# Kernel optimization log

Hardware: AMD Instinct MI355X
Metric: run time of the kernel (lower is better)

## Reference

```python
import jax, jax.numpy as jnp
import numpy as np

R = 12          # resolution (H = W = G); L = R**3 = 1728
HEADS = 12


def setup_inputs() -> dict:
    key = jax.random.key(0)
    k1, k2, k3 = jax.random.split(key, 3)
    B, L, C = 4, R ** 3, 768
    qkv = jax.random.normal(k1, (3, B, L, C), dtype=jnp.float32)
    lepe_w = jax.random.normal(k2, (C, 1, 3, 3, 3), dtype=jnp.float32) * 0.05
    lepe_b = jax.random.normal(k3, (C,), dtype=jnp.float32) * 0.01
    return {"qkv": qkv, "lepe_w": lepe_w, "lepe_b": lepe_b}


def reference(qkv, lepe_w, lepe_b):
    # qkv: [3, B, L, C]; idx=0 => window == full volume, so attention is dense over L.
    q, k, v = qkv[0], qkv[1], qkv[2]
    B, L, C = q.shape
    hd = C // HEADS
    scale = hd ** -0.5

    # im2cswin with full-volume window preserves token order: [B, L, C] -> [B, H, L, d]
    qh = q.reshape(B, L, HEADS, hd).transpose(0, 2, 1, 3)
    kh = k.reshape(B, L, HEADS, hd).transpose(0, 2, 1, 3)

    # get_lepe: v -> [B, C, R, R, R], depthwise 3x3x3 conv (groups=C)
    v_img = v.transpose(0, 2, 1).reshape(B, C, R, R, R)
    lepe = jax.lax.conv_general_dilated(
        v_img, lepe_w, window_strides=(1, 1, 1), padding="SAME",
        dimension_numbers=("NCDHW", "OIDHW", "NCDHW"), feature_group_count=C,
    ) + lepe_b[None, :, None, None, None]
    lepe = lepe.reshape(B, HEADS, hd, L).transpose(0, 1, 3, 2)   # [B, H, L, d]
    vh = v_img.reshape(B, HEADS, hd, L).transpose(0, 1, 3, 2)    # [B, H, L, d]

    attn = jax.nn.softmax(jnp.einsum("bhqd,bhkd->bhqk", qh * scale, kh), axis=-1)
    out = jnp.einsum("bhqk,bhkd->bhqd", attn, vh) + lepe          # [B, H, L, d]

    # windows2img with full window is an inverse reshape back to [B, L, C]
    return out.transpose(0, 2, 1, 3).reshape(B, L, C)
```

## Files before the change

kernel.cpp:

```cpp
#include <hip/hip_runtime.h>

#define RR 12
#define LL 1728
#define CC 768
#define HEADS 12
#define HD 64
#define BATCH 4

typedef __attribute__((ext_vector_type(8))) short bf8;
typedef __attribute__((ext_vector_type(4))) float f4;

__device__ inline unsigned short f2bf(float x) {
  unsigned int u = __float_as_uint(x);
  return (unsigned short)((u + 0x7FFFu + ((u >> 16) & 1u)) >> 16);
}
__device__ inline unsigned short f2bfr(float x) {
  return (unsigned short)((__float_as_uint(x) + 0x8000u) >> 16);
}

__device__ inline float fast_exp2(float x) {
#if __has_builtin(__builtin_amdgcn_exp2f)
  return __builtin_amdgcn_exp2f(x);
#else
  return exp2f(x);
#endif
}

__device__ inline void gld16(const unsigned short* g, unsigned short* l) {
  __builtin_amdgcn_global_load_lds((const __attribute__((address_space(1))) unsigned int*)g,
                                   (__attribute__((address_space(3))) unsigned int*)l, 16, 0, 0);
}

#define QSCALE 0.1803368801111244f

#define NLEPE 5184
#define NPREP 1296

__global__ __launch_bounds__(256) void combined_kernel(const float* __restrict__ qkv,
                                                       const float* __restrict__ w,
                                                       const float* __restrict__ bias,
                                                       unsigned short* __restrict__ qb,
                                                       unsigned short* __restrict__ kb,
                                                       unsigned short* __restrict__ vT,
                                                       float* __restrict__ out) {
  __shared__ __align__(16) unsigned char smem[27648];
  const int bid = blockIdx.x;
  const int t = threadIdx.x;

  if (bid < NLEPE) {
    const int xg = (bid % 3) * 4;
    const int line = (bid / 3) % 144;
    const int ct = (bid / 432) % 3;
    const int b = bid / 1296;
    const int z = line / RR;
    const int y = line % RR;
    const int c0 = ct * 256;
    const int c = c0 + t;
    float* w_lds = (float*)smem;

    {
      const float* wsrc = w + (size_t)c0 * 27;
#pragma unroll
      for (int i = 0; i < 7; ++i) {
        const int idx = i * 256 + t;
        if (idx < 1728) *(float4*)&w_lds[idx * 4] = *(const float4*)&wsrc[idx * 4];
      }
    }
    __syncthreads();
    float wreg[27];
#pragma unroll
    for (int j = 0; j < 27; ++j) wreg[j] = w_lds[t * 27 + j];

    const float* vb = qkv + ((size_t)(2 * BATCH + b)) * LL * CC + c;
    const float bv = bias[c];
    float acc[4] = {bv, bv, bv, bv};

#pragma unroll
    for (int dz = -1; dz <= 1; ++dz) {
#pragma unroll
      for (int dy = -1; dy <= 1; ++dy) {
        const int zz = z + dz, yy = y + dy;
        const bool lineok = ((unsigned)zz < RR) & ((unsigned)yy < RR);
        const int base = (zz * RR + yy) * RR;
        float v6[6];
#pragma unroll
        for (int p = 0; p < 6; ++p) {
          const int xx = xg - 1 + p;
          const bool ok = lineok & ((unsigned)xx < RR);
          const int lp = ok ? base + xx : 0;
          const float vv = vb[(size_t)lp * CC];
          v6[p] = ok ? vv : 0.f;
        }
        const int jb = ((dz + 1) * 3 + (dy + 1)) * 3;
        const float wL = wreg[jb], wC = wreg[jb + 1], wR = wreg[jb + 2];
#pragma unroll
        for (int i = 0; i < 4; ++i)
          acc[i] += wL * v6[i] + wC * v6[i + 1] + wR * v6[i + 2];
      }
    }
    const size_t obase = ((size_t)b * LL + line * RR + xg) * CC + c;
#pragma unroll
    for (int i = 0; i < 4; ++i) out[obase + (size_t)i * CC] = acc[i];

  } else {
    const int p = bid - NLEPE;
    const int lt = p % 27;
    const int h = (p / 27) % HEADS;
    const int b = p / (27 * HEADS);
    unsigned short* tl = (unsigned short*)smem;

    {
      const int r0 = t >> 4;
      const int c4 = (t & 15) * 4;
#pragma unroll
      for (int pi = 0; pi < 4; ++pi) {
        const int row = lt * 64 + pi * 16 + r0;
        const size_t off = ((size_t)b * LL + row) * CC + h * HD + c4;
        const float4 qv = *(const float4*)(qkv + off);
        ushort4 oq;
        oq.x = f2bf(qv.x * QSCALE); oq.y = f2bf(qv.y * QSCALE);
        oq.z = f2bf(qv.z * QSCALE); oq.w = f2bf(qv.w * QSCALE);
        *(ushort4*)(qb + off) = oq;
        const float4 kv = *(const float4*)(qkv + (size_t)BATCH * LL * CC + off);
        ushort4 ok;
        ok.x = f2bf(kv.x); ok.y = f2bf(kv.y); ok.z = f2bf(kv.z); ok.w = f2bf(kv.w);
        *(ushort4*)(kb + off) = ok;
      }
    }

    const float* vsrc = qkv + ((size_t)(2 * BATCH + b)) * LL * CC;
#pragma unroll
    for (int it = 0; it < 4; ++it) {
      const int idx = it * 256 + t;
      const int lrow = idx >> 4;
      const int c4 = (idx & 15) * 4;
      const float4 vv = *(const float4*)(vsrc + (size_t)(lt * 64 + lrow) * CC + h * HD + c4);
      tl[(c4 + 0) * 65 + lrow] = f2bf(vv.x);
      tl[(c4 + 1) * 65 + lrow] = f2bf(vv.y);
      tl[(c4 + 2) * 65 + lrow] = f2bf(vv.z);
      tl[(c4 + 3) * 65 + lrow] = f2bf(vv.w);
    }
    __syncthreads();
#pragma unroll
    for (int it = 0; it < 4; ++it) {
      const int idx = it * 256 + t;
      const int drow = idx >> 4;
      const int u = idx & 15;
      const int s4 = u * 4;
      const int kbase = (((u >> 3) * 2 + (u & 1)) << 4) + (((u >> 1) & 3) << 2);
      ushort4 o;
      o.x = tl[drow * 65 + kbase + 0];
      o.y = tl[drow * 65 + kbase + 1];
      o.z = tl[drow * 65 + kbase + 2];
      o.w = tl[drow * 65 + kbase + 3];
      *(ushort4*)(vT + (((size_t)(b * HEADS + h) * HD + drow) * LL) + lt * 64 + s4) = o;
    }
  }
}

__global__ __launch_bounds__(512, 4) void attn_kernel(const unsigned short* __restrict__ qb,
                                                      const unsigned short* __restrict__ kb,
                                                      const unsigned short* __restrict__ vT,
                                                      float* __restrict__ out) {
  __shared__ unsigned short k_lds[3][64 * 64];
  __shared__ unsigned short v_lds[3][64 * 64];

  const int g = blockIdx.x;
  const int xcd = g & 7;
  const int ix = g >> 3;
  const int qt = ix % 7;
  const int bh = xcd * 6 + ix / 7;
  const int h = bh % HEADS;
  const int b = bh / HEADS;
  const int stg = (qt * 4) % 27;

  const int t = threadIdx.x;
  const int lane = t & 63;
  const int wave = t >> 6;
  const int m = lane & 15;
  const int quad = lane >> 4;

  bf8 qf[2][2];
#pragma unroll
  for (int sub = 0; sub < 2; ++sub) {
    int row = qt * 256 + sub * 128 + wave * 16 + m;
    row = row < LL ? row : LL - 1;
    const size_t qbase = ((size_t)(b * LL + row)) * CC + h * HD;
    qf[sub][0] = *(const bf8*)(qb + qbase + quad * 8);
    qf[sub][1] = *(const bf8*)(qb + qbase + 32 + quad * 8);
  }

  int koff, voff, ldsb;
  {
    const int cidx = wave * 64 + lane;
    const int row = cidx >> 3;
    const int sc = (cidx & 7) ^ (row & 7);
    koff = row * CC + sc * 8;
    voff = row * LL + sc * 8;
    ldsb = wave * 512;
  }

  const unsigned short* kgb = kb + (size_t)b * LL * CC + h * HD;
  const unsigned short* vgb = vT + ((size_t)(b * HEADS + h) * HD) * LL;

#define ISSUE_TILE(KT, BUF)                                                             \
  {                                                                                     \
    gld16(kgb + (size_t)(KT) * (64 * CC) + koff, &k_lds[BUF][ldsb]);                    \
    gld16(vgb + (KT) * 64 + voff, &v_lds[BUF][ldsb]);                                   \
  }

  ISSUE_TILE(stg, 0)
  {
    int k1 = stg + 1; if (k1 >= 27) k1 -= 27;
    ISSUE_TILE(k1, 1)
  }

  f4 o_acc[2][4] = {};
  float psum[2] = {0.f, 0.f};

#define ATTN_BODY(I, STG, WAITN, DOISSUE)                                               \
  {                                                                                     \
    __asm__ volatile("s_waitcnt vmcnt(" #WAITN ")" ::: "memory");                       \
    __builtin_amdgcn_s_barrier();                                                       \
    if (DOISSUE) {                                                                      \
      int ktn = stg + (I) + 2; if (ktn >= 27) ktn -= 27;                                \
      ISSUE_TILE(ktn, ((STG) + 2) % 3)                                                  \
    }                                                                                   \
    f4 s_acc[2][4] = {};                                                                \
    __builtin_amdgcn_s_setprio(1);                                                      \
    _Pragma("unroll")                                                                   \
    for (int nt = 0; nt < 4; ++nt) {                                                    \
      _Pragma("unroll")                                                                 \
      for (int ks = 0; ks < 2; ++ks) {                                                  \
        const int cc = ((ks * 4 + quad) ^ (m & 7)) * 8;                                 \
        const bf8 kf = *(const bf8*)&k_lds[STG][(nt * 16 + m) * 64 + cc];               \
        s_acc[0][nt] = __builtin_amdgcn_mfma_f32_16x16x32_bf16(kf, qf[0][ks], s_acc[0][nt], 0, 0, 0); \
        s_acc[1][nt] = __builtin_amdgcn_mfma_f32_16x16x32_bf16(kf, qf[1][ks], s_acc[1][nt], 0, 0, 0); \
      }                                                                                 \
    }                                                                                   \
    __builtin_amdgcn_s_setprio(0);                                                      \
    bf8 pf[2][2];                                                                       \
    _Pragma("unroll")                                                                   \
    for (int sub = 0; sub < 2; ++sub) {                                                 \
      _Pragma("unroll")                                                                 \
      for (int ks = 0; ks < 2; ++ks) {                                                  \
        union { bf8 v; unsigned int w[4]; } pu;                                         \
        _Pragma("unroll")                                                               \
        for (int bb = 0; bb < 2; ++bb) {                                                \
          const int nt = ks * 2 + bb;                                                   \
          const float p0 = fast_exp2(s_acc[sub][nt][0]);                                \
          const float p1 = fast_exp2(s_acc[sub][nt][1]);                                \
          const float p2 = fast_exp2(s_acc[sub][nt][2]);                                \
          const float p3 = fast_exp2(s_acc[sub][nt][3]);                                \
          psum[sub] += (p0 + p1) + (p2 + p3);                                           \
          pu.w[bb * 2 + 0] = (unsigned int)f2bfr(p0) | ((unsigned int)f2bfr(p1) << 16); \
          pu.w[bb * 2 + 1] = (unsigned int)f2bfr(p2) | ((unsigned int)f2bfr(p3) << 16); \
        }                                                                               \
        pf[sub][ks] = pu.v;                                                             \
      }                                                                                 \
    }                                                                                   \
    __builtin_amdgcn_s_setprio(1);                                                      \
    _Pragma("unroll")                                                                   \
    for (int nt = 0; nt < 4; ++nt) {                                                    \
      _Pragma("unroll")                                                                 \
      for (int ks = 0; ks < 2; ++ks) {                                                  \
        const int cc = ((ks * 4 + quad) ^ (m & 7)) * 8;                                 \
        const bf8 vf = *(const bf8*)&v_lds[STG][(nt * 16 + m) * 64 + cc];               \
        o_acc[0][nt] = __builtin_amdgcn_mfma_f32_16x16x32_bf16(vf, pf[0][ks], o_acc[0][nt], 0, 0, 0); \
        o_acc[1][nt] = __builtin_amdgcn_mfma_f32_16x16x32_bf16(vf, pf[1][ks], o_acc[1][nt], 0, 0, 0); \
      }                                                                                 \
    }                                                                                   \
    __builtin_amdgcn_s_setprio(0);                                                      \
  }

  for (int ip = 0; ip < 8; ++ip) {
    const int i0 = ip * 3;
    ATTN_BODY(i0 + 0, 0, 2, true)
    ATTN_BODY(i0 + 1, 1, 2, true)
    ATTN_BODY(i0 + 2, 2, 2, true)
  }
  ATTN_BODY(24, 0, 2, true)
  ATTN_BODY(25, 1, 2, false)
  ATTN_BODY(26, 2, 0, false)
#undef ATTN_BODY
#undef ISSUE_TILE

#pragma unroll
  for (int sub = 0; sub < 2; ++sub) {
    float s = psum[sub];
    s += __shfl_xor(s, 16);
    s += __shfl_xor(s, 32);
    const float inv = 1.0f / s;
    const int rowq = qt * 256 + sub * 128 + wave * 16 + m;
    if (rowq < LL) {
      float* op = out + ((size_t)b * LL + rowq) * CC + h * HD + quad * 4;
#pragma unroll
      for (int nt = 0; nt < 4; ++nt) {
        float4 o4 = *(float4*)&op[nt * 16];
        o4.x += o_acc[sub][nt][0] * inv;
        o4.y += o_acc[sub][nt][1] * inv;
        o4.z += o_acc[sub][nt][2] * inv;
        o4.w += o_acc[sub][nt][3] * inv;
        *(float4*)&op[nt * 16] = o4;
      }
    }
  }
}

extern "C" void kernel_launch(void* const* d_in, const int* in_sizes, int n_in,
                              void* d_out, int out_size, void* d_ws, size_t ws_size,
                              hipStream_t stream) {
  (void)in_sizes; (void)n_in; (void)ws_size; (void)out_size;
  const float* qkv = (const float*)d_in[0];
  const float* lepe_w = (const float*)d_in[1];
  const float* lepe_b = (const float*)d_in[2];
  float* out = (float*)d_out;

  const size_t NE = (size_t)BATCH * LL * CC;
  unsigned short* qb = (unsigned short*)d_ws;
  unsigned short* kb = qb + NE;
  unsigned short* vT = kb + NE;

  combined_kernel<<<dim3(NLEPE + NPREP), 256, 0, stream>>>(qkv, lepe_w, lepe_b, qb, kb, vT, out);
  attn_kernel<<<dim3(336), 512, 0, stream>>>(qb, kb, vT, out);
}
```

Baseline: 191.3 us.

## Split key tiles across wave halves and reduce partial outputs in LDS

Each block now handles 128 query rows instead of 256. The two halves of its 8 waves each process 32 of the 64 keys in every tile, and their partial output accumulators and row sums are combined through shared memory at the end. This doubles the grid to 672 blocks, cuts per-wave register use, and raises launch_bounds occupancy to 6, aiming to fill more CUs and hide latency better. In exchange it adds an LDS reduction with an extra barrier, and each K/V tile is loaded twice as often across the grid.

```diff
diff --git a/kernel.cpp b/kernel.cpp
--- a/kernel.cpp
+++ b/kernel.cpp
@@ -158,7 +158,7 @@
   }
 }
 
-__global__ __launch_bounds__(512, 4) void attn_kernel(const unsigned short* __restrict__ qb,
+__global__ __launch_bounds__(512, 6) void attn_kernel(const unsigned short* __restrict__ qb,
                                                       const unsigned short* __restrict__ kb,
                                                       const unsigned short* __restrict__ vT,
                                                       float* __restrict__ out) {
@@ -168,26 +168,28 @@
   const int g = blockIdx.x;
   const int xcd = g & 7;
   const int ix = g >> 3;
-  const int qt = ix % 7;
-  const int bh = xcd * 6 + ix / 7;
+  const int qt = ix % 14;
+  const int bh = xcd * 6 + ix / 14;
   const int h = bh % HEADS;
   const int b = bh / HEADS;
-  const int stg = (qt * 4) % 27;
+  const int stg = (qt * 2) % 27;
 
   const int t = threadIdx.x;
   const int lane = t & 63;
   const int wave = t >> 6;
   const int m = lane & 15;
   const int quad = lane >> 4;
+  const int half = wave >> 2;
+  const int qg = wave & 3;
 
   bf8 qf[2][2];
 #pragma unroll
-  for (int sub = 0; sub < 2; ++sub) {
-    int row = qt * 256 + sub * 128 + wave * 16 + m;
+  for (int qsub = 0; qsub < 2; ++qsub) {
+    int row = qt * 128 + qg * 32 + qsub * 16 + m;
     row = row < LL ? row : LL - 1;
     const size_t qbase = ((size_t)(b * LL + row)) * CC + h * HD;
-    qf[sub][0] = *(const bf8*)(qb + qbase + quad * 8);
-    qf[sub][1] = *(const bf8*)(qb + qbase + 32 + quad * 8);
+    qf[qsub][0] = *(const bf8*)(qb + qbase + quad * 8);
+    qf[qsub][1] = *(const bf8*)(qb + qbase + 32 + quad * 8);
   }
 
   int koff, voff, ldsb;
@@ -215,7 +217,7 @@
     ISSUE_TILE(k1, 1)
   }
 
-  f4 o_acc[2][4] = {};
+  f4 o_acc[4][2] = {};
   float psum[2] = {0.f, 0.f};
 
 #define ATTN_BODY(I, STG, WAITN, DOISSUE)                                               \
@@ -226,49 +228,42 @@
       int ktn = stg + (I) + 2; if (ktn >= 27) ktn -= 27;                                \
       ISSUE_TILE(ktn, ((STG) + 2) % 3)                                                  \
     }                                                                                   \
-    f4 s_acc[2][4] = {};                                                                \
+    f4 s_acc[2][2] = {};                            \
     __builtin_amdgcn_s_setprio(1);                                                      \
     _Pragma("unroll")                                                                   \
-    for (int nt = 0; nt < 4; ++nt) {                                                    \
+    for (int knt = 0; knt < 2; ++knt) {                                                 \
       _Pragma("unroll")                                                                 \
-      for (int ks = 0; ks < 2; ++ks) {                                                  \
-        const int cc = ((ks * 4 + quad) ^ (m & 7)) * 8;                                 \
-        const bf8 kf = *(const bf8*)&k_lds[STG][(nt * 16 + m) * 64 + cc];               \
-        s_acc[0][nt] = __builtin_amdgcn_mfma_f32_16x16x32_bf16(kf, qf[0][ks], s_acc[0][nt], 0, 0, 0); \
-        s_acc[1][nt] = __builtin_amdgcn_mfma_f32_16x16x32_bf16(kf, qf[1][ks], s_acc[1][nt], 0, 0, 0); \
+      for (int ksd = 0; ksd < 2; ++ksd) {                                               \
+        const int cc = ((ksd * 4 + quad) ^ (m & 7)) * 8;                                \
+        const bf8 kf = *(const bf8*)&k_lds[STG][(half * 32 + knt * 16 + m) * 64 + cc];  \
+        s_acc[knt][0] = __builtin_amdgcn_mfma_f32_16x16x32_bf16(kf, qf[0][ksd], s_acc[knt][0], 0, 0, 0); \
+        s_acc[knt][1] = __builtin_amdgcn_mfma_f32_16x16x32_bf16(kf, qf[1][ksd], s_acc[knt][1], 0, 0, 0); \
       }                                                                                 \
     }                                                                                   \
     __builtin_amdgcn_s_setprio(0);                                                      \
-    bf8 pf[2][2];                                                                       \
+    bf8 pf[2];          \
     _Pragma("unroll")                                                                   \
-    for (int sub = 0; sub < 2; ++sub) {                                                 \
+    for (int qsub = 0; qsub < 2; ++qsub) {                                              \
+      union { bf8 v; unsigned int w[4]; } pu;                                           \
       _Pragma("unroll")                                                                 \
-      for (int ks = 0; ks < 2; ++ks) {                                                  \
-        union { bf8 v; unsigned int w[4]; } pu;                                         \
-        _Pragma("unroll")                                                               \
-        for (int bb = 0; bb < 2; ++bb) {                                                \
-          const int nt = ks * 2 + bb;                                                   \
-          const float p0 = fast_exp2(s_acc[sub][nt][0]);                                \
-          const float p1 = fast_exp2(s_acc[sub][nt][1]);                                \
-          const float p2 = fast_exp2(s_acc[sub][nt][2]);                                \
-          const float p3 = fast_exp2(s_acc[sub][nt][3]);                                \
-          psum[sub] += (p0 + p1) + (p2 + p3);                                           \
-          pu.w[bb * 2 + 0] = (unsigned int)f2bfr(p0) | ((unsigned int)f2bfr(p1) << 16); \
-          pu.w[bb * 2 + 1] = (unsigned int)f2bfr(p2) | ((unsigned int)f2bfr(p3) << 16); \
-        }                                                                               \
-        pf[sub][ks] = pu.v;                                                             \
+      for (int knt = 0; knt < 2; ++knt) {                                               \
+        const float p0 = fast_exp2(s_acc[knt][qsub][0]);                                \
+        const float p1 = fast_exp2(s_acc[knt][qsub][1]);                                \
+        const float p2 = fast_exp2(s_acc[knt][qsub][2]);                                \
+        const float p3 = fast_exp2(s_acc[knt][qsub][3]);                                \
+        psum[qsub] += (p0 + p1) + (p2 + p3);                                            \
+        pu.w[knt * 2 + 0] = (unsigned int)f2bfr(p0) | ((unsigned int)f2bfr(p1) << 16);  \
+        pu.w[knt * 2 + 1] = (unsigned int)f2bfr(p2) | ((unsigned int)f2bfr(p3) << 16);  \
       }                                                                                 \
+      pf[qsub] = pu.v;                                                                  \
     }                                                                                   \
     __builtin_amdgcn_s_setprio(1);                                                      \
     _Pragma("unroll")                                                                   \
     for (int nt = 0; nt < 4; ++nt) {                                                    \
-      _Pragma("unroll")                                                                 \
-      for (int ks = 0; ks < 2; ++ks) {                                                  \
-        const int cc = ((ks * 4 + quad) ^ (m & 7)) * 8;                                 \
-        const bf8 vf = *(const bf8*)&v_lds[STG][(nt * 16 + m) * 64 + cc];               \
-        o_acc[0][nt] = __builtin_amdgcn_mfma_f32_16x16x32_bf16(vf, pf[0][ks], o_acc[0][nt], 0, 0, 0); \
-        o_acc[1][nt] = __builtin_amdgcn_mfma_f32_16x16x32_bf16(vf, pf[1][ks], o_acc[1][nt], 0, 0, 0); \
-      }                                                                                 \
+      const int cc = ((half * 4 + quad) ^ (m & 7)) * 8;                                 \
+      const bf8 vf = *(const bf8*)&v_lds[STG][(nt * 16 + m) * 64 + cc];                 \
+      o_acc[nt][0] = __builtin_amdgcn_mfma_f32_16x16x32_bf16(vf, pf[0], o_acc[nt][0], 0, 0, 0); \
+      o_acc[nt][1] = __builtin_amdgcn_mfma_f32_16x16x32_bf16(vf, pf[1], o_acc[nt][1], 0, 0, 0); \
     }                                                                                   \
     __builtin_amdgcn_s_setprio(0);                                                      \
   }
@@ -285,22 +280,49 @@
 #undef ATTN_BODY
 #undef ISSUE_TILE
 
-#pragma unroll
-  for (int sub = 0; sub < 2; ++sub) {
-    float s = psum[sub];
+  __syncthreads();
+  {
+    float* red = (float*)&k_lds[0][0];
+    const int sid = qg * 64 + lane;
+    float* slot = red + sid * 36;
+    if (half == 1) {
+#pragma unroll
+      for (int qsub = 0; qsub < 2; ++qsub) {
+#pragma unroll
+        for (int nt = 0; nt < 4; ++nt)
+          *(f4*)(slot + (qsub * 4 + nt) * 4) = o_acc[nt][qsub];
+        slot[32 + qsub] = psum[qsub];
+      }
+    }
+    __syncthreads();
+    if (half == 1) return;
+#pragma unroll
+    for (int qsub = 0; qsub < 2; ++qsub) {
+#pragma unroll
+      for (int nt = 0; nt < 4; ++nt) {
+        const f4 po = *(const f4*)(slot + (qsub * 4 + nt) * 4);
+        o_acc[nt][qsub] += po;
+      }
+      psum[qsub] += slot[32 + qsub];
+    }
+  }
+
+#pragma unroll
+  for (int qsub = 0; qsub < 2; ++qsub) {
+    float s = psum[qsub];
     s += __shfl_xor(s, 16);
     s += __shfl_xor(s, 32);
     const float inv = 1.0f / s;
-    const int rowq = qt * 256 + sub * 128 + wave * 16 + m;
+    const int rowq = qt * 128 + qg * 32 + qsub * 16 + m;
     if (rowq < LL) {
       float* op = out + ((size_t)b * LL + rowq) * CC + h * HD + quad * 4;
 #pragma unroll
       for (int nt = 0; nt < 4; ++nt) {
         float4 o4 = *(float4*)&op[nt * 16];
-        o4.x += o_acc[sub][nt][0] * inv;
-        o4.y += o_acc[sub][nt][1] * inv;
-        o4.z += o_acc[sub][nt][2] * inv;
-        o4.w += o_acc[sub][nt][3] * inv;
+        o4.x += o_acc[nt][qsub][0] * inv;
+        o4.y += o_acc[nt][qsub][1] * inv;
+        o4.z += o_acc[nt][qsub][2] * inv;
+        o4.w += o_acc[nt][qsub][3] * inv;
         *(float4*)&op[nt * 16] = o4;
       }
     }
@@ -322,5 +344,5 @@
   unsigned short* vT = kb + NE;
 
   combined_kernel<<<dim3(NLEPE + NPREP), 256, 0, stream>>>(qkv, lepe_w, lepe_b, qb, kb, vT, out);
-  attn_kernel<<<dim3(336), 512, 0, stream>>>(qb, kb, vT, out);
-}
+  attn_kernel<<<dim3(672), 512, 0, stream>>>(qb, kb, vT, out);
+}
```

Measured after the change: 370.9 us. 93.9% more time.
